# Optimization experiments

Hardware: AMD Instinct MI355X
Metric: run time of the kernel (lower is better)

## Reference

```python
import jax, jax.numpy as jnp
import numpy as np

DILATIONS = (3, 6, 12, 18, 24)
B, C, H, W = 16, 26, 96, 72
INNER = 128
EPS = 1e-5


def conv2d(x, w, padding=0, dilation=1):
    return jax.lax.conv_general_dilated(
        x, w, window_strides=(1, 1),
        padding=[(padding, padding), (padding, padding)],
        rhs_dilation=(dilation, dilation),
        dimension_numbers=('NCHW', 'OIHW', 'NCHW'))


def batch_norm(x, p):
    # p: [4, C] rows = (scale, bias, running_mean, running_var); eval-mode BN
    s, b, m, v = p[0], p[1], p[2], p[3]
    inv = s * jax.lax.rsqrt(v + EPS)
    return x * inv[None, :, None, None] + (b - m * inv)[None, :, None, None]


def basic_block(x, w1, p1, w2, p2, wd=None, pd=None):
    h = jax.nn.relu(batch_norm(conv2d(x, w1, padding=1), p1))
    h = batch_norm(conv2d(h, w2, padding=1), p2)
    idn = x if wd is None else batch_norm(conv2d(x, wd), pd)
    return jax.nn.relu(h + idn)


def _bilinear(img, py, px):
    # img: [cpg, H, W]; py, px: [K, H, W] sample coords; zero outside bounds
    Hi, Wi = img.shape[1], img.shape[2]
    y0f = jnp.floor(py); x0f = jnp.floor(px)
    ly = py - y0f; lx = px - x0f
    y0 = y0f.astype(jnp.int32); x0 = x0f.astype(jnp.int32)

    def gather(yi, xi):
        valid = ((yi >= 0) & (yi < Hi) & (xi >= 0) & (xi < Wi)).astype(img.dtype)
        return img[:, jnp.clip(yi, 0, Hi - 1), jnp.clip(xi, 0, Wi - 1)] * valid[None]

    return (gather(y0, x0) * ((1 - ly) * (1 - lx))[None]
            + gather(y0, x0 + 1) * ((1 - ly) * lx)[None]
            + gather(y0 + 1, x0) * (ly * (1 - lx))[None]
            + gather(y0 + 1, x0 + 1) * (ly * lx)[None])


def deform_conv(x, offset, w, dil):
    # x: [B,C,H,W]; offset: [B, dg*2*K, H, W] ((dy,dx) interleaved per kernel tap);
    # w: [O,C,3,3]; stride 1, padding = dil -> same spatial size
    Bn, Cn, Hn, Wn = x.shape
    K = w.shape[2] * w.shape[3]
    dg = offset.shape[1] // (2 * K)
    cpg = Cn // dg
    off = offset.reshape(Bn, dg, K, 2, Hn, Wn)
    ky = jnp.arange(K) // 3 - 1
    kx = jnp.arange(K) % 3 - 1
    base_y = (jnp.arange(Hn)[None, :] + ky[:, None] * dil).astype(x.dtype)  # [K,H]
    base_x = (jnp.arange(Wn)[None, :] + kx[:, None] * dil).astype(x.dtype)  # [K,W]
    py = base_y[None, None, :, :, None] + off[:, :, :, 0]  # [B,dg,K,H,W]
    px = base_x[None, None, :, None, :] + off[:, :, :, 1]
    xg = x.reshape(Bn, dg, cpg, Hn, Wn)
    samp = jax.vmap(jax.vmap(_bilinear))(xg, py, px)  # [B,dg,cpg,K,H,W]
    vals = samp.reshape(Bn, Cn, K, Hn, Wn)
    return jnp.einsum('bckij,ock->boij', vals, w.reshape(w.shape[0], Cn, K))


def setup_inputs():
    key = jax.random.key(0)
    ks = jax.random.split(key, 14)
    std = 0.001  # matches nn.init.normal_(std=0.001)

    def bnp(k, c):
        k1, k2, k3, k4 = jax.random.split(k, 4)
        return jnp.stack([jax.random.uniform(k1, (c,), minval=0.5, maxval=1.5),
                          jax.random.normal(k2, (c,)) * 0.1,
                          jax.random.normal(k3, (c,)) * 0.1,
                          jax.random.uniform(k4, (c,), minval=0.5, maxval=1.5)])

    return {
        'ref_x': jax.random.normal(ks[0], (B, C, H, W), jnp.float32),
        'sup_x': jax.random.normal(ks[1], (B, C, H, W), jnp.float32),
        'w1_0': jax.random.normal(ks[2], (INNER, C, 3, 3), jnp.float32) * std,
        'w2_0': jax.random.normal(ks[3], (INNER, INNER, 3, 3), jnp.float32) * std,
        'wd_0': jax.random.normal(ks[4], (INNER, C, 1, 1), jnp.float32) * std,
        'bn1_0': bnp(ks[5], INNER),
        'bn2_0': bnp(ks[6], INNER),
        'bnd_0': bnp(ks[7], INNER),
        'w1_rest': jax.random.normal(ks[8], (19, INNER, INNER, 3, 3), jnp.float32) * std,
        'w2_rest': jax.random.normal(ks[9], (19, INNER, INNER, 3, 3), jnp.float32) * std,
        'bn1_rest': jnp.stack([bnp(k, INNER) for k in jax.random.split(ks[10], 19)]),
        'bn2_rest': jnp.stack([bnp(k, INNER) for k in jax.random.split(ks[11], 19)]),
        'offset_ws': jax.random.normal(ks[12], (5, C * 2 * 9, INNER, 3, 3), jnp.float32) * std,
        'deform_ws': jax.random.normal(ks[13], (5, C, C, 3, 3), jnp.float32) * std,
    }


def reference(ref_x, sup_x, w1_0, w2_0, wd_0, bn1_0, bn2_0, bnd_0,
              w1_rest, w2_rest, bn1_rest, bn2_rest, offset_ws, deform_ws):
    # offset feature chain: 20 BasicBlocks on (ref - sup)
    h = basic_block(ref_x - sup_x, w1_0, bn1_0, w2_0, bn2_0, wd_0, bnd_0)
    for t in range(19):
        h = basic_block(h, w1_rest[t], bn1_rest[t], w2_rest[t], bn2_rest[t])
    # 5 dilation branches: dilated offset conv -> deformable conv on sup_x; average
    out = jnp.zeros_like(sup_x)
    for i, dil in enumerate(DILATIONS):
        off = conv2d(h, offset_ws[i], padding=dil, dilation=dil)
        out = out + deform_conv(sup_x, off, deform_ws[i], dil)
    return out / len(DILATIONS)
```

## Files before the change

### kernel.cpp

```cpp
#include <hip/hip_runtime.h>

typedef unsigned short u16;
typedef unsigned int u32;
typedef __bf16 bf16x8 __attribute__((ext_vector_type(8)));
typedef float f32x4 __attribute__((ext_vector_type(4)));

#define NB 16
#define CIN 26
#define IMH 96
#define IMW 72
#define HW6912 6912
#define NPIX 110592
#define SPH 98
#define SPW 74
#define SPAD 1

__device__ __forceinline__ float b2f(u16 h) {
    union { u32 u; float f; } x; x.u = ((u32)h) << 16; return x.f;
}
__device__ __forceinline__ u16 f2b(float f) {
    union { float f; u32 u; } x; x.f = f;
    u32 u = x.u;
    u32 r = (u + 0x7fffu + ((u >> 16) & 1u)) >> 16;
    return (u16)r;
}
__device__ __forceinline__ float ldin(const void* p, int i, int f) {
    return f ? ((const float*)p)[i] : b2f(((const u16*)p)[i]);
}

__device__ __forceinline__ int pbase(int m, int clog2) {
    int b = m / HW6912;
    int p = m - b * HW6912;
    int y = p / IMW;
    int x = p - y * IMW;
    return (((b * SPH + y + SPAD) * SPW) + (x + SPAD)) << clog2;
}

__device__ __forceinline__ void glds16(const u16* g, u16* l) {
    __builtin_amdgcn_global_load_lds(
        (const __attribute__((address_space(1))) void*)g,
        (__attribute__((address_space(3))) void*)l, 16, 0, 0);
}

__global__ void probe_kernel(const void* bn, int* flag) {
    if (threadIdx.x == 0 && blockIdx.x == 0) {
        const float* f = (const float*)bn;
        int cnt = 0;
        for (int j = 64; j < 128; ++j) {
            float v = f[j];
            if (v >= 0.4f && v <= 1.6f) cnt++;
        }
        *flag = (cnt >= 32) ? 1 : 0;
    }
}

__global__ __launch_bounds__(256) void zero_ws_kernel(uint4* p, int n16) {
    int i = blockIdx.x * 256 + threadIdx.x;
    int stride = gridDim.x * 256;
    for (; i < n16; i += stride) p[i] = make_uint4(0u, 0u, 0u, 0u);
}

__global__ __launch_bounds__(256) void fill_x0_kernel(const void* __restrict__ ref,
                                                      const void* __restrict__ sup,
                                                      u16* __restrict__ x0,
                                                      const int* __restrict__ flag) {
    int f = *flag;
    int t = blockIdx.x * 256 + threadIdx.x;
    int b = t / HW6912;
    int p = t - b * HW6912;
    int y = p / IMW;
    int x = p - y * IMW;
    int dst = ((b * SPH + y + SPAD) * SPW + (x + SPAD)) << 5;
    #pragma unroll 1
    for (int c = 0; c < CIN; ++c) {
        int src = (b * CIN + c) * HW6912 + p;
        x0[dst + c] = f2b(ldin(ref, src, f) - ldin(sup, src, f));
    }
}

__global__ __launch_bounds__(256) void prep_rest_kernel(const void* __restrict__ w1r,
                                                        const void* __restrict__ w2r,
                                                        const void* __restrict__ bn1r,
                                                        const void* __restrict__ bn2r,
                                                        u16* __restrict__ dst,
                                                        const int* __restrict__ flag) {
    int f = *flag;
    int idx = blockIdx.x * 256 + threadIdx.x;
    int c = idx / 147456;
    int e = idx - c * 147456;
    int ee = e & 7;
    int l = (e >> 3) & 63;
    int j = (e >> 9) & 1;
    int w2 = (e >> 10) & 1;
    int rest = e >> 11;
    int it = rest % 36;
    int nt = rest / 36;
    int n = nt * 64 + w2 * 32 + j * 16 + (l & 15);
    int k = it * 32 + ((l >> 4) << 3) + ee;
    int s = k >> 7, ci = k & 127;
    const void* w  = (c < 19) ? w1r : w2r;
    int wb         = ((c < 19) ? c : (c - 19)) * 147456;
    const void* bn = (c < 19) ? bn1r : bn2r;
    int bb         = ((c < 19) ? c : (c - 19)) * 512;
    float inv = ldin(bn, bb + n, f) * rsqrtf(ldin(bn, bb + 384 + n, f) + 1e-5f);
    dst[idx] = f2b(ldin(w, wb + (n * 128 + ci) * 9 + s, f) * inv);
}

__global__ __launch_bounds__(256) void prep_b0_kernel(const void* __restrict__ w1_0,
                                                      const void* __restrict__ w2_0,
                                                      const void* __restrict__ wd_0,
                                                      const void* __restrict__ bn1_0,
                                                      const void* __restrict__ bn2_0,
                                                      const void* __restrict__ bnd_0,
                                                      u16* __restrict__ W20,
                                                      u16* __restrict__ W10,
                                                      u16* __restrict__ Wd,
                                                      const int* __restrict__ flag) {
    int f = *flag;
    int idx = blockIdx.x * 256 + threadIdx.x;
    if (idx < 147456) {
        int e = idx;
        int ee = e & 7;
        int l = (e >> 3) & 63;
        int j = (e >> 9) & 1;
        int w2 = (e >> 10) & 1;
        int rest = e >> 11;
        int it = rest % 36;
        int nt = rest / 36;
        int n = nt * 64 + w2 * 32 + j * 16 + (l & 15);
        int k = it * 32 + ((l >> 4) << 3) + ee;
        int s = k >> 7, ci = k & 127;
        float inv = ldin(bn2_0, n, f) * rsqrtf(ldin(bn2_0, 384 + n, f) + 1e-5f);
        W20[idx] = f2b(ldin(w2_0, (n * 128 + ci) * 9 + s, f) * inv);
    } else if (idx < 184320) {
        int j = idx - 147456;
        int o = j / 288, k = j - o * 288;
        int s = k >> 5, ci = k & 31;
        float inv = ldin(bn1_0, o, f) * rsqrtf(ldin(bn1_0, 384 + o, f) + 1e-5f);
        W10[j] = (ci < CIN) ? f2b(ldin(w1_0, (o * CIN + ci) * 9 + s, f) * inv) : (u16)0;
    } else {
        int j = idx - 184320;
        int o = j >> 5, ci = j & 31;
        float inv = ldin(bnd_0, o, f) * rsqrtf(ldin(bnd_0, 384 + o, f) + 1e-5f);
        Wd[j] = (ci < CIN) ? f2b(ldin(wd_0, o * CIN + ci, f) * inv) : (u16)0;
    }
}

__global__ __launch_bounds__(256) void prep_off_kernel(const void* __restrict__ offw,
                                                       u16* __restrict__ dst,
                                                       const int* __restrict__ flag) {
    int f = *flag;
    int idx = blockIdx.x * 256 + threadIdx.x;
    int e = idx & 7;
    int l = (idx >> 3) & 63;
    int j = (idx >> 9) & 1;
    int w2 = (idx >> 10) & 1;
    int rest = idx >> 11;
    int it = rest % 36;
    int dnt = rest / 36;
    int nt = dnt & 7;
    int d = dnt >> 3;
    int n = nt * 64 + w2 * 32 + j * 16 + (l & 15);
    int k = it * 32 + (l >> 4) * 8 + e;
    int s = k >> 7, ci = k & 127;
    dst[idx] = (n < 468) ? f2b(ldin(offw, ((d * 468 + n) * 128 + ci) * 9 + s, f)) : (u16)0;
}

__global__ __launch_bounds__(256) void prep_dw_kernel(const void* __restrict__ dwall,
                                                      float* __restrict__ dst,
                                                      const int* __restrict__ flag) {
    int f = *flag;
    int idx = blockIdx.x * 256 + threadIdx.x;
    if (idx >= 32760) return;
    int d = idx / 6552;
    int r = idx - d * 6552;
    int o = r % 28;
    int ct = r / 28;
    int c = ct / 9, t = ct - c * 9;
    dst[idx] = (o < CIN) ? ldin(dwall, d * 6084 + (o * CIN + c) * 9 + t, f) : 0.f;
}

__global__ __launch_bounds__(256) void prep_bias_kernel(const void* __restrict__ bn1_0,
                                                        const void* __restrict__ bn2_0,
                                                        const void* __restrict__ bnd_0,
                                                        const void* __restrict__ bn1r,
                                                        const void* __restrict__ bn2r,
                                                        float* __restrict__ dst,
                                                        const int* __restrict__ flag) {
    int f = *flag;
    int idx = blockIdx.x * 256 + threadIdx.x;
    if (idx >= 41 * 128) return;
    int set = idx >> 7;
    int o = idx & 127;
    const void* bn; int bb = 0;
    if (set == 0) bn = bn1_0;
    else if (set == 1) bn = bn2_0;
    else if (set == 2) bn = bnd_0;
    else if (set < 22) { bn = bn1r; bb = (set - 3) * 512; }
    else { bn = bn2r; bb = (set - 22) * 512; }
    float s = ldin(bn, bb + o, f), b = ldin(bn, bb + 128 + o, f);
    float mu = ldin(bn, bb + 256 + o, f), v = ldin(bn, bb + 384 + o, f);
    float inv = s * rsqrtf(v + 1e-5f);
    dst[idx] = b - mu * inv;
}

__global__ __launch_bounds__(256) void conv_gemm(const u16* __restrict__ A,
                                                 const u16* __restrict__ W,
                                                 const float* __restrict__ bias,
                                                 u16* __restrict__ out,
                                                 int clog2, int nslab, int K,
                                                 int relu) {
    __shared__ u16 As[2][128 * 32];
    __shared__ u16 Bs[2][64 * 32];
    int tid = threadIdx.x;
    int m0 = blockIdx.x * 128;
    int n0 = blockIdx.y * 64;
    int Cin = 1 << clog2;

    int r0 = tid >> 2;
    int q8 = (tid & 3) * 8;
    int arow0 = pbase(m0 + r0, clog2) + q8;
    int arow1 = pbase(m0 + r0 + 64, clog2) + q8;
    int brow0 = (n0 + r0) * K + q8;
    int l8 = tid * 8;

    f32x4 acc[4][2];
    #pragma unroll
    for (int i = 0; i < 4; ++i)
        #pragma unroll
        for (int j = 0; j < 2; ++j)
            acc[i][j] = (f32x4){0.f, 0.f, 0.f, 0.f};

    int wid = tid >> 6;
    int wm = (wid >> 1) * 64;
    int wn = (wid & 1) * 32;
    int lane = tid & 63;
    int lr = lane & 15;
    int lq = lane >> 4;

    int nk = K >> 5;
    auto stage = [&](int buf, int kt) {
        int sl = kt >> clog2;
        int win = kt & (Cin - 1);
        int soff = 0;
        if (nslab == 9) {
            int d3 = sl / 3;
            soff = (((d3 - 1) * SPW + (sl - d3 * 3 - 1))) << clog2;
        }
        glds16(A + arow0 + soff + win, &As[buf][l8]);
        glds16(A + arow1 + soff + win, &As[buf][2048 + l8]);
        glds16(W + brow0 + kt, &Bs[buf][l8]);
    };

    stage(0, 0);
    #pragma unroll 1
    for (int it = 0; it < nk; ++it) {
        __syncthreads();
        if (it + 1 < nk) stage((it + 1) & 1, (it + 1) << 5);
        const u16* as = As[it & 1];
        const u16* bs = Bs[it & 1];
        bf16x8 af[4], bfr[2];
        #pragma unroll
        for (int i = 0; i < 4; ++i)
            af[i] = *(const bf16x8*)&as[(wm + i * 16 + lr) * 32 + lq * 8];
        #pragma unroll
        for (int j = 0; j < 2; ++j)
            bfr[j] = *(const bf16x8*)&bs[(wn + j * 16 + lr) * 32 + lq * 8];
        #pragma unroll
        for (int i = 0; i < 4; ++i)
            #pragma unroll
            for (int j = 0; j < 2; ++j)
                acc[i][j] = __builtin_amdgcn_mfma_f32_16x16x32_bf16(af[i], bfr[j], acc[i][j], 0, 0, 0);
    }

    #pragma unroll
    for (int i = 0; i < 4; ++i) {
        #pragma unroll
        for (int r = 0; r < 4; ++r) {
            int ml = m0 + wm + i * 16 + lq * 4 + r;
            int ob = pbase(ml, 7);
            #pragma unroll
            for (int j = 0; j < 2; ++j) {
                int n = n0 + wn + j * 16 + lr;
                float v = acc[i][j][r] + bias[n];
                if (relu) v = fmaxf(v, 0.f);
                out[ob + n] = f2b(v);
            }
        }
    }
}

__global__ __launch_bounds__(256, 4) void chain_conv(const u16* __restrict__ A,
                                                     const u16* __restrict__ W,
                                                     const float* __restrict__ bias,
                                                     const u16* __restrict__ idn,
                                                     u16* __restrict__ out,
                                                     int relu) {
    __shared__ u16 As[2][2][128 * 32];
    int tid = threadIdx.x;
    int wg = blockIdx.x;
    int mt = (wg & 7) * 108 + (wg >> 3);
    int m0 = mt * 128;

    int r0 = tid >> 2;
    int c8 = ((tid & 3) ^ (r0 & 3)) * 8;
    int pbq[2];
    #pragma unroll
    for (int q = 0; q < 2; ++q) {
        int p = m0 + r0 + q * 64;
        int b = p / HW6912;
        int rem = p - b * HW6912;
        int y = rem / IMW;
        int x = rem - y * IMW;
        pbq[q] = ((b * SPH + y + 1) * SPW + (x + 1)) * 128 + c8;
    }
    int l8 = tid * 8;

    f32x4 acc[4][4];
    #pragma unroll
    for (int i = 0; i < 4; ++i)
        #pragma unroll
        for (int jj = 0; jj < 4; ++jj)
            acc[i][jj] = (f32x4){0.f, 0.f, 0.f, 0.f};

    int wid = tid >> 6;
    int wm = (wid >> 1) * 64;
    int wn2 = wid & 1;
    int lane = tid & 63;
    int lr = lane & 15;
    int lq = lane >> 4;
    int rchunk = (lq ^ (lr & 3)) * 8;

    const u16* wv = W + wn2 * 73728 + lane * 8;

    auto stageh = [&](int buf, int it36) {
        int kt = it36 << 5;
        int sl = kt >> 7;
        int win = kt & 127;
        int d3 = sl / 3;
        int soff = ((d3 - 1) * SPW + (sl - d3 * 3 - 1)) * 128;
        glds16(A + pbq[0] + soff + win, &As[buf][it36 & 1][l8]);
        glds16(A + pbq[1] + soff + win, &As[buf][it36 & 1][2048 + l8]);
    };

    bf16x8 bcur[4], bnxt[4];
    #pragma unroll
    for (int jj = 0; jj < 4; ++jj)
        bcur[jj] = *(const bf16x8*)(wv + jj * 512);

    stageh(0, 0);
    stageh(0, 1);
    #pragma unroll
    for (int it = 0; it < 18; ++it) {
        __syncthreads();
        if (it + 1 < 18) {
            stageh((it + 1) & 1, (it + 1) * 2);
            stageh((it + 1) & 1, (it + 1) * 2 + 1);
        }
        #pragma unroll
        for (int kc = 0; kc < 2; ++kc) {
            int it36 = it * 2 + kc;
            if (it36 + 1 < 36) {
                #pragma unroll
                for (int jj = 0; jj < 4; ++jj)
                    bnxt[jj] = *(const bf16x8*)(wv + (it36 + 1) * 2048 + jj * 512);
            }
            const u16* as = As[it & 1][kc];
            bf16x8 af[4];
            #pragma unroll
            for (int i = 0; i < 4; ++i)
                af[i] = *(const bf16x8*)&as[(wm + i * 16 + lr) * 32 + rchunk];
            #pragma unroll
            for (int i = 0; i < 4; ++i)
                #pragma unroll
                for (int jj = 0; jj < 4; ++jj)
                    acc[i][jj] = __builtin_amdgcn_mfma_f32_16x16x32_bf16(af[i], bcur[jj], acc[i][jj], 0, 0, 0);
            if (it36 + 1 < 36) {
                #pragma unroll
                for (int jj = 0; jj < 4; ++jj)
                    bcur[jj] = bnxt[jj];
            }
        }
    }

    #pragma unroll
    for (int i = 0; i < 4; ++i) {
        #pragma unroll
        for (int r = 0; r < 4; ++r) {
            int ml = m0 + wm + i * 16 + lq * 4 + r;
            int ob = pbase(ml, 7);
            #pragma unroll
            for (int jj = 0; jj < 4; ++jj) {
                int n = wn2 * 64 + jj * 16 + lr;
                float v = acc[i][jj][r] + bias[n];
                if (idn) v += b2f(idn[ob + n]);
                if (relu) v = fmaxf(v, 0.f);
                out[ob + n] = f2b(v);
            }
        }
    }
}

__global__ __launch_bounds__(256, 8) void off_conv(const u16* __restrict__ A,
                                                   const u16* __restrict__ W,
                                                   u16* __restrict__ out,
                                                   int dil, int m_base) {
    __shared__ u16 As[2][128 * 32];
    int tid = threadIdx.x;
    int wg = blockIdx.x;
    int sw = (wg & 7) * 216 + (wg >> 3);
    int mt = sw >> 3, nt = sw & 7;
    int m0 = mt * 128, n0 = nt * 64;

    int r0 = tid >> 2;
    int q8 = (tid & 3) * 8;
    int pb2[2], py[2], px[2];
    #pragma unroll
    for (int q = 0; q < 2; ++q) {
        int p = m_base + m0 + r0 + q * 64;
        int b = p / HW6912;
        int rem = p - b * HW6912;
        pb2[q] = b;
        py[q] = rem / IMW;
        px[q] = rem - py[q] * IMW;
    }
    int l8 = tid * 8;

    f32x4 acc[4][2];
    #pragma unroll
    for (int i = 0; i < 4; ++i) {
        acc[i][0] = (f32x4){0.f, 0.f, 0.f, 0.f};
        acc[i][1] = (f32x4){0.f, 0.f, 0.f, 0.f};
    }

    int wid = tid >> 6;
    int wm = (wid >> 1) * 64;
    int wn = (wid & 1) * 32;
    int lane = tid & 63;
    int lr = lane & 15;
    int lq = lane >> 4;

    const u16* wv = W + nt * 73728 + (wid & 1) * 1024 + lane * 8;

    auto stage = [&](int buf, int kt) {
        int sl = kt >> 7;
        int win = kt & 127;
        int d3 = sl / 3;
        int dy = (d3 - 1) * dil, dx = (sl - d3 * 3 - 1) * dil;
        #pragma unroll
        for (int q = 0; q < 2; ++q) {
            int y2 = py[q] + dy, x2 = px[q] + dx;
            uint4 v = make_uint4(0u, 0u, 0u, 0u);
            if (y2 >= 0 && y2 < IMH && x2 >= 0 && x2 < IMW)
                v = *(const uint4*)(A + ((pb2[q] * SPH + y2 + 1) * SPW + x2 + 1) * 128 + win + q8);
            *(uint4*)&As[buf][q * 2048 + l8] = v;
        }
    };

    stage(0, 0);
    #pragma unroll 1
    for (int it = 0; it < 36; ++it) {
        __syncthreads();
        if (it + 1 < 36) stage((it + 1) & 1, (it + 1) << 5);
        const u16* as = As[it & 1];
        bf16x8 af[4], bfr[2];
        #pragma unroll
        for (int i = 0; i < 4; ++i)
            af[i] = *(const bf16x8*)&as[(wm + i * 16 + lr) * 32 + lq * 8];
        bfr[0] = *(const bf16x8*)(wv + it * 2048);
        bfr[1] = *(const bf16x8*)(wv + it * 2048 + 512);
        #pragma unroll
        for (int i = 0; i < 4; ++i)
            #pragma unroll
            for (int j = 0; j < 2; ++j)
                acc[i][j] = __builtin_amdgcn_mfma_f32_16x16x32_bf16(af[i], bfr[j], acc[i][j], 0, 0, 0);
    }

    #pragma unroll
    for (int i = 0; i < 4; ++i) {
        #pragma unroll
        for (int r = 0; r < 4; ++r) {
            int ml = m0 + wm + i * 16 + lq * 4 + r;
            int ob = ml * 468;
            #pragma unroll
            for (int j = 0; j < 2; ++j) {
                int n = n0 + wn + j * 16 + lr;
                if (n < 468) out[ob + n] = f2b(acc[i][j][r]);
            }
        }
    }
}

template <int F>
__device__ __forceinline__ float dsamp2(const void* sup, int base, int yi, int xi) {
    bool ok = (yi >= 0) & (yi < IMH) & (xi >= 0) & (xi < IMW);
    int yc = yi < 0 ? 0 : (yi > IMH - 1 ? IMH - 1 : yi);
    int xc = xi < 0 ? 0 : (xi > IMW - 1 ? IMW - 1 : xi);
    float v = F ? ((const float*)sup)[base + yc * IMW + xc]
                : b2f(((const u16*)sup)[base + yc * IMW + xc]);
    return ok ? v : 0.f;
}

template <int F>
__device__ __forceinline__ void deform_body(const void* __restrict__ sup,
                                            const u16* __restrict__ oc,
                                            const float* __restrict__ wsm,
                                            f32x4 acc[7],
                                            int c0, int c1, int b, int y, int x, int dil) {
    #pragma unroll 1
    for (int c = c0; c < c1; ++c) {
        int ibase = (b * CIN + c) * HW6912;
        #pragma unroll
        for (int t = 0; t < 9; ++t) {
            u32 pr = *(const u32*)(oc + c * 18 + t * 2);
            float dy = b2f((u16)(pr & 0xffffu));
            float dx = b2f((u16)(pr >> 16));
            float py = (float)(y + (t / 3 - 1) * dil) + dy;
            float px = (float)(x + (t % 3 - 1) * dil) + dx;
            float y0f = floorf(py), x0f = floorf(px);
            float ly = py - y0f, lx = px - x0f;
            int y0 = (int)y0f, x0 = (int)x0f;
            float v00 = dsamp2<F>(sup, ibase, y0, x0);
            float v01 = dsamp2<F>(sup, ibase, y0, x0 + 1);
            float v10 = dsamp2<F>(sup, ibase, y0 + 1, x0);
            float v11 = dsamp2<F>(sup, ibase, y0 + 1, x0 + 1);
            float val = (v00 * (1.f - lx) + v01 * lx) * (1.f - ly)
                      + (v10 * (1.f - lx) + v11 * lx) * ly;
            const float4* wr = (const float4*)&wsm[(c * 9 + t) * 28];
            #pragma unroll
            for (int u = 0; u < 7; ++u) {
                float4 w4 = wr[u];
                acc[u][0] = fmaf(val, w4.x, acc[u][0]);
                acc[u][1] = fmaf(val, w4.y, acc[u][1]);
                acc[u][2] = fmaf(val, w4.z, acc[u][2]);
                acc[u][3] = fmaf(val, w4.w, acc[u][3]);
            }
        }
    }
}

__global__ __launch_bounds__(256) void deform_kernel(const void* __restrict__ sup,
                                                     const u16* __restrict__ offb,
                                                     const float* __restrict__ wsp,
                                                     float* __restrict__ accws,
                                                     int dil, int first, int m_base,
                                                     const int* __restrict__ flag) {
    int f = *flag;
    __shared__ alignas(16) float wsm[26 * 9 * 28];
    __shared__ float red[4 * 32 * 27];
    int tid = threadIdx.x;
    int bid = blockIdx.x;
    int sw = (bid & 7) * 108 + (bid >> 3);
    for (int i = tid; i < 1638; i += 256)
        ((float4*)wsm)[i] = ((const float4*)wsp)[i];
    __syncthreads();

    int px = tid & 31;
    int cg = tid >> 5;
    int c0 = (cg * 26) >> 3;
    int c1 = ((cg + 1) * 26) >> 3;
    int ml = sw * 32 + px;
    int m = m_base + ml;
    int b = m / HW6912;
    int p = m - b * HW6912;
    int y = p / IMW;
    int x = p - y * IMW;

    f32x4 acc[7];
    #pragma unroll
    for (int u = 0; u < 7; ++u) acc[u] = (f32x4){0.f, 0.f, 0.f, 0.f};

    const u16* oc = offb + (size_t)ml * 468;
    if (f) deform_body<1>(sup, oc, wsm, acc, c0, c1, b, y, x, dil);
    else   deform_body<0>(sup, oc, wsm, acc, c0, c1, b, y, x, dil);

    #pragma unroll
    for (int u = 0; u < 7; ++u)
        #pragma unroll
        for (int k2 = 0; k2 < 4; ++k2) {
            float v = acc[u][k2];
            acc[u][k2] = v + __shfl_xor(v, 32);
        }

    int w = tid >> 6;
    if (!(tid & 32)) {
        float* mr = red + (w * 32 + px) * 27;
        #pragma unroll
        for (int u = 0; u < 7; ++u)
            #pragma unroll
            for (int k2 = 0; k2 < 4; ++k2) {
                int o = u * 4 + k2;
                if (o < 26) mr[o] = acc[u][k2];
            }
    }
    __syncthreads();

    int base_m = m_base + sw * 32;
    for (int v = tid; v < 32 * 26; v += 256) {
        int ppx = v / 26;
        int o = v - ppx * 26;
        float s = red[(0 * 32 + ppx) * 27 + o] + red[(1 * 32 + ppx) * 27 + o]
                + red[(2 * 32 + ppx) * 27 + o] + red[(3 * 32 + ppx) * 27 + o];
        size_t ai = (size_t)(base_m + ppx) * 32 + o;
        if (first) accws[ai] = s;
        else       accws[ai] += s;
    }
}

__global__ __launch_bounds__(256) void finalize_kernel(const float* __restrict__ accws,
                                                       void* __restrict__ out,
                                                       const int* __restrict__ flag) {
    int f = *flag;
    int q = blockIdx.x * 256 + threadIdx.x;
    int b = q / (CIN * HW6912);
    int r = q - b * (CIN * HW6912);
    int o = r / HW6912;
    int p = r - o * HW6912;
    float v = accws[(size_t)(b * HW6912 + p) * 32 + o] * 0.2f;
    if (f) ((float*)out)[q] = v;
    else   ((u16*)out)[q] = f2b(v);
}

extern "C" void kernel_launch(void* const* d_in, const int* in_sizes, int n_in,
                              void* d_out, int out_size, void* d_ws, size_t ws_size,
                              hipStream_t stream) {
    (void)in_sizes; (void)n_in; (void)out_size;
    const void* ref_x    = d_in[0];
    const void* sup_x    = d_in[1];
    const void* w1_0     = d_in[2];
    const void* w2_0     = d_in[3];
    const void* wd_0     = d_in[4];
    const void* bn1_0    = d_in[5];
    const void* bn2_0    = d_in[6];
    const void* bnd_0    = d_in[7];
    const void* w1_rest  = d_in[8];
    const void* w2_rest  = d_in[9];
    const void* bn1_rest = d_in[10];
    const void* bn2_rest = d_in[11];
    const void* offset_w = d_in[12];
    const void* deform_w = d_in[13];

    size_t o_x0    = 0;
    size_t o_h0    = o_x0 + 7426048;
    size_t o_h1s   = o_h0 + 29704192;
    size_t o_acc   = o_h1s + 29704192;
    size_t o_wrest = o_acc + 14155776;
    size_t o_w20   = o_wrest + 11206656;
    size_t o_w10   = o_w20 + 294912;
    size_t o_wd    = o_w10 + 73728;
    size_t o_woff  = o_wd + 8192;
    size_t o_bias  = o_woff + 5898240;
    size_t o_wsall = o_bias + 20992;
    size_t o_flag  = o_wsall + 131072;
    size_t o_end   = o_flag + 64;
    if (ws_size < o_end) return;

    char* ws = (char*)d_ws;
    u16* x0    = (u16*)(ws + o_x0);
    u16* h0    = (u16*)(ws + o_h0);
    u16* offb  = (u16*)(ws + o_h0);
    u16* h1s   = (u16*)(ws + o_h1s);
    float* accb = (float*)(ws + o_acc);
    u16* Wr    = (u16*)(ws + o_wrest);
    u16* W20   = (u16*)(ws + o_w20);
    u16* W10   = (u16*)(ws + o_w10);
    u16* Wd    = (u16*)(ws + o_wd);
    u16* Woff  = (u16*)(ws + o_woff);
    float* biasb = (float*)(ws + o_bias);
    float* wsall = (float*)(ws + o_wsall);
    int* flagp = (int*)(ws + o_flag);

    dim3 blk(256);

    probe_kernel<<<1, 64, 0, stream>>>(bn1_0, flagp);
    zero_ws_kernel<<<2048, blk, 0, stream>>>((uint4*)ws, (int)((7426048 + 2 * 29704192) / 16));
    fill_x0_kernel<<<432, blk, 0, stream>>>(ref_x, sup_x, x0, flagp);
    prep_rest_kernel<<<21888, blk, 0, stream>>>(w1_rest, w2_rest, bn1_rest, bn2_rest, Wr, flagp);
    prep_b0_kernel<<<736, blk, 0, stream>>>(w1_0, w2_0, wd_0, bn1_0, bn2_0, bnd_0, W20, W10, Wd, flagp);
    prep_off_kernel<<<11520, blk, 0, stream>>>(offset_w, Woff, flagp);
    prep_dw_kernel<<<128, blk, 0, stream>>>(deform_w, wsall, flagp);
    prep_bias_kernel<<<21, blk, 0, stream>>>(bn1_0, bn2_0, bnd_0, bn1_rest, bn2_rest, biasb, flagp);

    conv_gemm<<<dim3(864, 2), blk, 0, stream>>>(x0, Wd, biasb + 2 * 128, h1s, 5, 1, 32, 0);
    conv_gemm<<<dim3(864, 2), blk, 0, stream>>>(x0, W10, biasb + 0 * 128, h0, 5, 9, 288, 1);
    chain_conv<<<864, blk, 0, stream>>>(h0, W20, biasb + 1 * 128, h1s, h1s, 1);

    for (int t = 0; t < 19; ++t) {
        const u16* wa = Wr + (size_t)t * 147456;
        const u16* wb = Wr + (size_t)(19 + t) * 147456;
        chain_conv<<<864, blk, 0, stream>>>(h1s, wa, biasb + (3 + t) * 128, nullptr, h0, 1);
        chain_conv<<<864, blk, 0, stream>>>(h0, wb, biasb + (22 + t) * 128, h1s, h1s, 1);
    }

    const int dils[5] = {3, 6, 12, 18, 24};
    for (int i = 0; i < 5; ++i) {
        for (int cb = 0; cb < 4; ++cb) {
            int mb = cb * 27648;
            off_conv<<<1728, blk, 0, stream>>>(h1s, Woff + (size_t)i * 589824, offb, dils[i], mb);
            deform_kernel<<<864, blk, 0, stream>>>(sup_x, offb, wsall + (size_t)i * 6552,
                                                   accb, dils[i], (i == 0) ? 1 : 0, mb, flagp);
        }
    }
    finalize_kernel<<<11232, blk, 0, stream>>>(accb, d_out, flagp);
}
```

Measured before the change: 3.591 ms.

## Use four-slot LDS ring with prefetch depth two and explicit vmcnt waits in chain_conv

Replaces the double-buffered LDS pipeline with a 4-slot ring that stages each 32-wide K slice two iterations ahead. It drops __syncthreads in favour of hand-tuned s_waitcnt vmcnt counts plus s_barrier, so global-to-LDS loads can overlap with more MFMA work. The hand-counted vmcnt values are fragile: they depend on the compiler's exact ordering of vector memory ops, including the weight loads, and wrong counts would cause data races. A 4-slot ring also reuses a slot only two iterations after it was read, relying on the barrier for safety.

```diff
diff --git a/kernel.cpp b/kernel.cpp
--- a/kernel.cpp
+++ b/kernel.cpp
@@ -296,7 +296,7 @@
                                                      const u16* __restrict__ idn,
                                                      u16* __restrict__ out,
                                                      int relu) {
-    __shared__ u16 As[2][2][128 * 32];
+    __shared__ u16 As[4][128 * 32];
     int tid = threadIdx.x;
     int wg = blockIdx.x;
     int mt = (wg & 7) * 108 + (wg >> 3);
@@ -333,14 +333,14 @@
 
     const u16* wv = W + wn2 * 73728 + lane * 8;
 
-    auto stageh = [&](int buf, int it36) {
+    auto stage32 = [&](int it36) {
         int kt = it36 << 5;
         int sl = kt >> 7;
         int win = kt & 127;
         int d3 = sl / 3;
         int soff = ((d3 - 1) * SPW + (sl - d3 * 3 - 1)) * 128;
-        glds16(A + pbq[0] + soff + win, &As[buf][it36 & 1][l8]);
-        glds16(A + pbq[1] + soff + win, &As[buf][it36 & 1][2048 + l8]);
+        glds16(A + pbq[0] + soff + win, &As[it36 & 3][l8]);
+        glds16(A + pbq[1] + soff + win, &As[it36 & 3][2048 + l8]);
     };
 
     bf16x8 bcur[4], bnxt[4];
@@ -348,38 +348,37 @@
     for (int jj = 0; jj < 4; ++jj)
         bcur[jj] = *(const bf16x8*)(wv + jj * 512);
 
-    stageh(0, 0);
-    stageh(0, 1);
-    #pragma unroll
-    for (int it = 0; it < 18; ++it) {
-        __syncthreads();
-        if (it + 1 < 18) {
-            stageh((it + 1) & 1, (it + 1) * 2);
-            stageh((it + 1) & 1, (it + 1) * 2 + 1);
-        }
-        #pragma unroll
-        for (int kc = 0; kc < 2; ++kc) {
-            int it36 = it * 2 + kc;
-            if (it36 + 1 < 36) {
-                #pragma unroll
-                for (int jj = 0; jj < 4; ++jj)
-                    bnxt[jj] = *(const bf16x8*)(wv + (it36 + 1) * 2048 + jj * 512);
-            }
-            const u16* as = As[it & 1][kc];
-            bf16x8 af[4];
-            #pragma unroll
-            for (int i = 0; i < 4; ++i)
-                af[i] = *(const bf16x8*)&as[(wm + i * 16 + lr) * 32 + rchunk];
-            #pragma unroll
-            for (int i = 0; i < 4; ++i)
-                #pragma unroll
-                for (int jj = 0; jj < 4; ++jj)
-                    acc[i][jj] = __builtin_amdgcn_mfma_f32_16x16x32_bf16(af[i], bcur[jj], acc[i][jj], 0, 0, 0);
-            if (it36 + 1 < 36) {
-                #pragma unroll
-                for (int jj = 0; jj < 4; ++jj)
-                    bcur[jj] = bnxt[jj];
-            }
+    stage32(0);
+    stage32(1);
+    #pragma unroll
+    for (int it = 0; it < 36; ++it) {
+        if (it + 2 < 36) stage32(it + 2);
+        if (it == 0)       asm volatile("s_waitcnt vmcnt(4)" ::: "memory");
+        else if (it == 1)  asm volatile("s_waitcnt vmcnt(8)" ::: "memory");
+        else if (it == 34) asm volatile("s_waitcnt vmcnt(10)" ::: "memory");
+        else if (it == 35) asm volatile("s_waitcnt vmcnt(8)" ::: "memory");
+        else               asm volatile("s_waitcnt vmcnt(12)" ::: "memory");
+        __builtin_amdgcn_s_barrier();
+        __builtin_amdgcn_sched_barrier(0);
+        if (it + 1 < 36) {
+            #pragma unroll
+            for (int jj = 0; jj < 4; ++jj)
+                bnxt[jj] = *(const bf16x8*)(wv + (it + 1) * 2048 + jj * 512);
+        }
+        const u16* as = As[it & 3];
+        bf16x8 af[4];
+        #pragma unroll
+        for (int i = 0; i < 4; ++i)
+            af[i] = *(const bf16x8*)&as[(wm + i * 16 + lr) * 32 + rchunk];
+        #pragma unroll
+        for (int i = 0; i < 4; ++i)
+            #pragma unroll
+            for (int jj = 0; jj < 4; ++jj)
+                acc[i][jj] = __builtin_amdgcn_mfma_f32_16x16x32_bf16(af[i], bcur[jj], acc[i][jj], 0, 0, 0);
+        if (it + 1 < 36) {
+            #pragma unroll
+            for (int jj = 0; jj < 4; ++jj)
+                bcur[jj] = bnxt[jj];
         }
     }
 
```

Result: slower. 3.687 ms (+2.7%).
